# Kernel tuning notes

Hardware: AMD Instinct MI355X
Metric: run time of the kernel (lower is better)

## Reference

```python
import jax, jax.numpy as jnp
import numpy as np

B, S, D = 2, 4096, 768
H = 12
HD = D // H  # 64
INNER = 4 * D
EPS = 1e-5


def setup_inputs() -> dict:
    key = jax.random.key(0)
    ks = jax.random.split(key, 12)
    sd = 0.02
    # causal additive mask (GPT-2 style): 0 where allowed, -1e9 where masked
    causal = jnp.tril(jnp.ones((S, S), dtype=bool))
    attention_mask = jnp.where(causal, 0.0, -1e9).astype(jnp.float32)[None, None]
    return {
        "hidden_states": jax.random.normal(ks[0], (B, S, D), dtype=jnp.float32),
        "attention_mask": attention_mask,
        "ln1_g": jnp.ones((D,), jnp.float32),
        "ln1_b": jnp.zeros((D,), jnp.float32),
        "w_attn": jax.random.normal(ks[1], (D, 3 * D), jnp.float32) * sd,
        "b_attn": jnp.zeros((3 * D,), jnp.float32),
        "w_cproj": jax.random.normal(ks[2], (D, D), jnp.float32) * sd,
        "b_cproj": jnp.zeros((D,), jnp.float32),
        "ln2_g": jnp.ones((D,), jnp.float32),
        "ln2_b": jnp.zeros((D,), jnp.float32),
        "w_fc": jax.random.normal(ks[3], (D, INNER), jnp.float32) * sd,
        "b_fc": jnp.zeros((INNER,), jnp.float32),
        "w_fc_proj": jax.random.normal(ks[4], (INNER, D), jnp.float32) * sd,
        "b_fc_proj": jnp.zeros((D,), jnp.float32),
    }


def _layernorm(x, g, b):
    mu = jnp.mean(x, axis=-1, keepdims=True)
    var = jnp.mean(jnp.square(x - mu), axis=-1, keepdims=True)
    return (x - mu) * jax.lax.rsqrt(var + EPS) * g + b


def reference(hidden_states, attention_mask, ln1_g, ln1_b, w_attn, b_attn,
              w_cproj, b_cproj, ln2_g, ln2_b, w_fc, b_fc, w_fc_proj, b_fc_proj):
    residual = hidden_states
    x = _layernorm(hidden_states, ln1_g, ln1_b)
    # qkv projection
    qkv = x @ w_attn + b_attn                       # [B,S,3D]
    q, k, v = jnp.split(qkv, 3, axis=-1)
    q = q.reshape(B, S, H, HD).transpose(0, 2, 1, 3)  # [B,H,S,HD]
    k = k.reshape(B, S, H, HD).transpose(0, 2, 1, 3)
    v = v.reshape(B, S, H, HD).transpose(0, 2, 1, 3)
    scale = HD ** -0.5
    scores = jnp.einsum('bhqd,bhkd->bhqk', q, k) * scale + attention_mask
    attn = jax.nn.softmax(scores, axis=-1)
    ctx = jnp.einsum('bhqk,bhkd->bhqd', attn, v)    # [B,H,S,HD]
    ctx = ctx.transpose(0, 2, 1, 3).reshape(B, S, D)
    attn_out = ctx @ w_cproj + b_cproj
    h = attn_out + residual
    residual = h
    y = _layernorm(h, ln2_g, ln2_b)
    y = jax.nn.gelu(y @ w_fc + b_fc, approximate=False)  # nn.GELU default = exact
    y = y @ w_fc_proj + b_fc_proj
    return y + residual
```

## Files before the change

kernel.cpp:

```cpp
#include <hip/hip_runtime.h>
#include <hip/hip_bf16.h>


#define S_     4096
#define D_     768
#define H_     12
#define HD_    64
#define NB_    2
#define M_     (NB_*S_)
#define QKV_   (3*D_)
#define INNER_ 3072

typedef unsigned short u16;
typedef __attribute__((ext_vector_type(4))) float f32x4;
typedef __attribute__((ext_vector_type(8))) short s16x8;

__device__ __forceinline__ float bf2f(u16 h) {
    union { unsigned int u; float f; } c; c.u = ((unsigned int)h) << 16; return c.f;
}
__device__ __forceinline__ u16 f2bf(float f) {
    union { float f; unsigned int u; } c; c.f = f;
    return (u16)((c.u + 0x7fffu + ((c.u >> 16) & 1u)) >> 16);
}
__device__ __forceinline__ void storev(u16* p, float v) { *p = f2bf(v); }
__device__ __forceinline__ void storev(float* p, float v) { *p = v; }

__device__ __forceinline__ float fexp2(float x) {
#if __has_builtin(__builtin_amdgcn_exp2f)
    return __builtin_amdgcn_exp2f(x);
#else
    return __expf(x * 0.69314718056f);
#endif
}
__device__ __forceinline__ unsigned int packbf(float a, float b) {
    union { __hip_bfloat162 h; unsigned int u; } c;
    c.h = __float22bfloat162_rn(float2{a, b});
    return c.u;
}

__device__ __forceinline__ void gload_lds16(const u16* g, u16* l) {
    __builtin_amdgcn_global_load_lds((const __attribute__((address_space(1))) void*)g,
                                     (__attribute__((address_space(3))) void*)l, 16, 0, 0);
}

#define WAITVM(N) asm volatile("s_waitcnt vmcnt(" #N ")" ::: "memory")

template <typename IT, bool PERM>
__global__ __launch_bounds__(256) void transpose_kernel(const IT* __restrict__ in,
                                                        u16* __restrict__ out,
                                                        int ld_in, int ld_out) {
    __shared__ u16 tile[32][33];
    const int c0 = blockIdx.x * 32, r0 = blockIdx.y * 32;
    const int tx = threadIdx.x & 31, ty = threadIdx.x >> 5;
#pragma unroll
    for (int i = 0; i < 32; i += 8) {
        IT v = in[(size_t)(r0 + ty + i) * ld_in + c0 + tx];
        u16 bv;
        if constexpr (sizeof(IT) == 4) bv = f2bf((float)v); else bv = (u16)v;
        tile[ty + i][tx] = bv;
    }
    __syncthreads();
    int oc = r0 + tx;
    if constexpr (PERM) oc = (oc & ~63) | (((oc & 15) << 2) | ((oc >> 4) & 3));
#pragma unroll
    for (int i = 0; i < 32; i += 8)
        out[(size_t)(c0 + ty + i) * ld_out + oc] = tile[tx][ty + i];
}

__global__ __launch_bounds__(256) void ln_row(const float* __restrict__ x, const float* __restrict__ g,
                                              const float* __restrict__ bb, u16* __restrict__ y,
                                              unsigned int* ctr) {
    const int row = blockIdx.x;
    const int tid = threadIdx.x;
    if (ctr && row == 0 && tid == 0) *ctr = 0u;
    const float* xr = x + (size_t)row * D_;
    float v0 = xr[tid], v1 = xr[tid + 256], v2 = xr[tid + 512];
    float s = v0 + v1 + v2, s2 = v0 * v0 + v1 * v1 + v2 * v2;
#pragma unroll
    for (int d = 32; d >= 1; d >>= 1) { s += __shfl_xor(s, d, 64); s2 += __shfl_xor(s2, d, 64); }
    __shared__ float red[8];
    const int wave = tid >> 6, lane = tid & 63;
    if (lane == 0) { red[wave] = s; red[4 + wave] = s2; }
    __syncthreads();
    s = red[0] + red[1] + red[2] + red[3];
    s2 = red[4] + red[5] + red[6] + red[7];
    const float mu = s * (1.0f / D_);
    const float var = s2 * (1.0f / D_) - mu * mu;
    const float rstd = rsqrtf(var + 1e-5f);
    u16* yr = y + (size_t)row * D_;
    yr[tid]       = f2bf((v0 - mu) * rstd * g[tid]       + bb[tid]);
    yr[tid + 256] = f2bf((v1 - mu) * rstd * g[tid + 256] + bb[tid + 256]);
    yr[tid + 512] = f2bf((v2 - mu) * rstd * g[tid + 512] + bb[tid + 512]);
}

template <int EPI, typename OT>
__global__ __launch_bounds__(256) void gemm_bt(const u16* __restrict__ A, const u16* __restrict__ Bt,
                                               const float* __restrict__ bias, const float* res,
                                               OT* C, int M, int N, int K) {
    __shared__ u16 As[3][128 * 32];
    __shared__ u16 Bs[3][128 * 32];
    const int tid = threadIdx.x;
    const int wave = tid >> 6, lane = tid & 63;
    const int m0 = blockIdx.y << 7, n0 = blockIdx.x << 7;
    const int fr = lane & 15, quad = lane >> 4;

    const int srow = wave * 16 + (lane >> 2);
    const int scol = (lane & 3) * 8;
    const u16* ag0 = A + (size_t)(m0 + srow) * K + scol;
    const u16* ag1 = ag0 + (size_t)64 * K;
    const u16* bg0 = Bt + (size_t)(n0 + srow) * K + scol;
    const u16* bg1 = bg0 + (size_t)64 * K;

    auto STAGE = [&](int k0, int b) {
        gload_lds16(ag0 + k0, &As[b][wave * 512]);
        gload_lds16(ag1 + k0, &As[b][2048 + wave * 512]);
        gload_lds16(bg0 + k0, &Bs[b][wave * 512]);
        gload_lds16(bg1 + k0, &Bs[b][2048 + wave * 512]);
    };

    const f32x4 fz = {0.f, 0.f, 0.f, 0.f};
    f32x4 acc[4][4];
#pragma unroll
    for (int i = 0; i < 4; i++)
#pragma unroll
        for (int j = 0; j < 4; j++) acc[i][j] = fz;

    const int wm = wave & 1, wn = wave >> 1;
    const int a_off = (wm * 64 + fr) * 32 + quad * 8;
    const int b_off = (wn * 64 + fr) * 32 + quad * 8;

    const int nsteps = K >> 5;
    STAGE(0, 0);
    if (nsteps > 1) { STAGE(32, 1); WAITVM(4); } else { WAITVM(0); }
    __syncthreads();

    for (int t = 0; t < nsteps; t++) {
        if (t + 2 < nsteps) STAGE((t + 2) << 5, (t + 2) % 3);
        const u16* a_rd = &As[t % 3][a_off];
        const u16* b_rd = &Bs[t % 3][b_off];
        s16x8 af[4], bfr[4];
#pragma unroll
        for (int u = 0; u < 4; u++) {
            af[u]  = *(const s16x8*)(a_rd + u * 16 * 32);
            bfr[u] = *(const s16x8*)(b_rd + u * 16 * 32);
        }
#pragma unroll
        for (int mt = 0; mt < 4; mt++)
#pragma unroll
            for (int nt = 0; nt < 4; nt++)
                acc[mt][nt] = __builtin_amdgcn_mfma_f32_16x16x32_bf16(af[mt], bfr[nt], acc[mt][nt], 0, 0, 0);
        if (t + 2 < nsteps) { WAITVM(4); } else { WAITVM(0); }
        __syncthreads();
    }

    const int crow0 = m0 + wm * 64 + quad * 4;
    const int ccol0 = n0 + wn * 64 + fr;
#pragma unroll
    for (int nt = 0; nt < 4; nt++) {
        const int col = ccol0 + nt * 16;
        const float bv = bias[col];
#pragma unroll
        for (int mt = 0; mt < 4; mt++) {
#pragma unroll
            for (int r = 0; r < 4; r++) {
                const int row = crow0 + mt * 16 + r;
                float v = acc[mt][nt][r] + bv;
                if constexpr (EPI == 1) v = 0.5f * v * (1.0f + erff(v * 0.70710678118654752f));
                if constexpr (EPI == 2) v += res[(size_t)row * N + col];
                storev(&C[(size_t)row * N + col], v);
            }
        }
    }
}

template <int EPI, typename OT>
__global__ __launch_bounds__(256) void gemm_bt64(const u16* __restrict__ A, const u16* __restrict__ Bt,
                                                 const float* __restrict__ bias, const float* res,
                                                 OT* C, int M, int N, int K) {
    __shared__ u16 As[3][128 * 32];
    __shared__ u16 Bs[3][64 * 32];
    const int tid = threadIdx.x;
    const int wave = tid >> 6, lane = tid & 63;
    const int m0 = blockIdx.y << 7, n0 = blockIdx.x << 6;
    const int fr = lane & 15, quad = lane >> 4;

    const int srow = wave * 16 + (lane >> 2);
    const int scol = (lane & 3) * 8;
    const u16* ag0 = A + (size_t)(m0 + srow) * K + scol;
    const u16* ag1 = ag0 + (size_t)64 * K;
    const u16* bg0 = Bt + (size_t)(n0 + srow) * K + scol;

    auto STAGE = [&](int k0, int b) {
        gload_lds16(ag0 + k0, &As[b][wave * 512]);
        gload_lds16(ag1 + k0, &As[b][2048 + wave * 512]);
        gload_lds16(bg0 + k0, &Bs[b][wave * 512]);
    };

    const f32x4 fz = {0.f, 0.f, 0.f, 0.f};
    f32x4 acc[2][4];
#pragma unroll
    for (int i = 0; i < 2; i++)
#pragma unroll
        for (int j = 0; j < 4; j++) acc[i][j] = fz;

    const int a_off = (wave * 32 + fr) * 32 + quad * 8;
    const int b_off = fr * 32 + quad * 8;

    const int nsteps = K >> 5;
    STAGE(0, 0);
    if (nsteps > 1) { STAGE(32, 1); WAITVM(3); } else { WAITVM(0); }
    __syncthreads();

    for (int t = 0; t < nsteps; t++) {
        if (t + 2 < nsteps) STAGE((t + 2) << 5, (t + 2) % 3);
        const u16* a_rd = &As[t % 3][a_off];
        const u16* b_rd = &Bs[t % 3][b_off];
        s16x8 af[2], bfr[4];
#pragma unroll
        for (int u = 0; u < 2; u++) af[u] = *(const s16x8*)(a_rd + u * 16 * 32);
#pragma unroll
        for (int u = 0; u < 4; u++) bfr[u] = *(const s16x8*)(b_rd + u * 16 * 32);
#pragma unroll
        for (int mt = 0; mt < 2; mt++)
#pragma unroll
            for (int nt = 0; nt < 4; nt++)
                acc[mt][nt] = __builtin_amdgcn_mfma_f32_16x16x32_bf16(af[mt], bfr[nt], acc[mt][nt], 0, 0, 0);
        if (t + 2 < nsteps) { WAITVM(3); } else { WAITVM(0); }
        __syncthreads();
    }

    const int crow0 = m0 + wave * 32 + quad * 4;
    const int ccol0 = n0 + fr;
#pragma unroll
    for (int nt = 0; nt < 4; nt++) {
        const int col = ccol0 + nt * 16;
        const float bv = bias[col];
#pragma unroll
        for (int mt = 0; mt < 2; mt++) {
#pragma unroll
            for (int r = 0; r < 4; r++) {
                const int row = crow0 + mt * 16 + r;
                float v = acc[mt][nt][r] + bv;
                if constexpr (EPI == 1) v = 0.5f * v * (1.0f + erff(v * 0.70710678118654752f));
                if constexpr (EPI == 2) v += res[(size_t)row * N + col];
                storev(&C[(size_t)row * N + col], v);
            }
        }
    }
}

#define SCALE_  0.1803368801111f
#define PST_    72
#define NITEMS_ (32 * H_ * NB_)
#define NWORK_  512
__global__ __launch_bounds__(256, 2) void flash_attn(const u16* __restrict__ qkv, const u16* __restrict__ vt,
                                                     u16* __restrict__ ctx, unsigned int* __restrict__ ctr) {
    const int tid = threadIdx.x;
    const int wave = tid >> 6, lane = tid & 63;
    const int fr = lane & 15, quad = lane >> 4;

    __shared__ u16 Ks[3][64 * 64];
    __shared__ u16 Vs[3][64 * 64];
    __shared__ u16 Ps4[4][32 * PST_];
    __shared__ int item_sh;
    u16* Ps = Ps4[wave];

    const int rsub = lane >> 3;
    const int schunk = ((lane & 7) ^ rsub) << 3;
    const int lds_woff = (wave << 4) * 64;

    const f32x4 fz = {0.f, 0.f, 0.f, 0.f};
    s16x8 ones;
#pragma unroll
    for (int j = 0; j < 8; j++) ones[j] = (short)0x3F80;

    for (;;) {
        if (tid == 0) item_sh = (int)atomicAdd(ctr, 1u);
        __syncthreads();
        const int item = item_sh;
        if (item >= NITEMS_) return;

        const int strip = 31 - item / (H_ * NB_);
        const int hb = item % (H_ * NB_);
        const int h = hb % H_, b = hb / H_;
        const int q0 = strip << 7;
        const int qwv = q0 + (wave << 5);

        const u16* Qg  = qkv + ((size_t)b * S_ + qwv) * QKV_ + h * HD_;
        const u16* Kg  = qkv + (size_t)b * S_ * QKV_ + D_ + h * HD_;
        const u16* Vtg = vt + ((size_t)b * D_ + h * HD_) * S_;
        const u16* KgS = Kg + (size_t)((wave << 4) + rsub) * QKV_ + schunk;
        const u16* VgS = Vtg + (size_t)((wave << 4) + rsub) * S_ + schunk;

        auto STAGEF = [&](int t, int bf) {
            const u16* kg = KgS + (size_t)(t << 6) * QKV_;
            const u16* vg = VgS + (t << 6);
            gload_lds16(kg, &Ks[bf][lds_woff]);
            gload_lds16(kg + (size_t)8 * QKV_, &Ks[bf][lds_woff + 512]);
            gload_lds16(vg, &Vs[bf][lds_woff]);
            gload_lds16(vg + (size_t)8 * S_, &Vs[bf][lds_woff + 512]);
        };

        s16x8 qf[2][2];
#pragma unroll
        for (int mt = 0; mt < 2; mt++)
#pragma unroll
            for (int kk = 0; kk < 2; kk++)
                qf[mt][kk] = *(const s16x8*)(Qg + (size_t)(mt * 16 + fr) * QKV_ + kk * 32 + quad * 8);

        f32x4 o[2][4];
        f32x4 ls[2];
#pragma unroll
        for (int mt = 0; mt < 2; mt++) {
            ls[mt] = fz;
#pragma unroll
            for (int nt = 0; nt < 4; nt++) o[mt][nt] = fz;
        }

        const int ntw = (strip << 1) + 2;

        STAGEF(0, 0);
        STAGEF(1, 1);
        WAITVM(4);
        __syncthreads();

        for (int t = 0; t < ntw; t++) {
            const int k0 = t << 6;

            if (t + 2 < ntw) STAGEF(t + 2, (t + 2) % 3);

            if (k0 <= qwv + 31) {
                const u16* kb = Ks[t % 3];
                const u16* vb = Vs[t % 3];

                s16x8 kc[2][4];
#pragma unroll
                for (int kk = 0; kk < 2; kk++)
#pragma unroll
                    for (int nt = 0; nt < 4; nt++) {
                        const int row = nt * 16 + fr;
                        const int sl = ((kk * 4 + quad) ^ (fr & 7)) << 3;
                        kc[kk][nt] = *(const s16x8*)(kb + row * 64 + sl);
                    }

                f32x4 sc[2][4];
#pragma unroll
                for (int mt = 0; mt < 2; mt++)
#pragma unroll
                    for (int nt = 0; nt < 4; nt++) sc[mt][nt] = fz;
                __builtin_amdgcn_s_setprio(1);
#pragma unroll
                for (int kk = 0; kk < 2; kk++)
#pragma unroll
                    for (int mt = 0; mt < 2; mt++)
#pragma unroll
                        for (int nt = 0; nt < 4; nt++)
                            sc[mt][nt] = __builtin_amdgcn_mfma_f32_16x16x32_bf16(qf[mt][kk], kc[kk][nt], sc[mt][nt], 0, 0, 0);
                __builtin_amdgcn_s_setprio(0);

                const bool fast = (k0 + 63 <= qwv);
#pragma unroll
                for (int mt = 0; mt < 2; mt++) {
#pragma unroll
                    for (int r = 0; r < 4; r++) {
                        float s0 = sc[mt][0][r] * SCALE_;
                        float s1 = sc[mt][1][r] * SCALE_;
                        float s2 = sc[mt][2][r] * SCALE_;
                        float s3 = sc[mt][3][r] * SCALE_;
                        if (!fast) {
                            const int lim = (qwv + mt * 16 + quad * 4 + r) - k0;
                            if (fr      > lim) s0 = -1e30f;
                            if (fr + 16 > lim) s1 = -1e30f;
                            if (fr + 32 > lim) s2 = -1e30f;
                            if (fr + 48 > lim) s3 = -1e30f;
                        }
                        s0 = fexp2(s0); s1 = fexp2(s1); s2 = fexp2(s2); s3 = fexp2(s3);
                        const int prow = mt * 16 + quad * 4 + r;
                        *(uint2*)(Ps + prow * PST_ + fr * 4) = make_uint2(packbf(s0, s1), packbf(s2, s3));
                    }
                }

                s16x8 vf[2][4];
#pragma unroll
                for (int kk = 0; kk < 2; kk++)
#pragma unroll
                    for (int nt = 0; nt < 4; nt++) {
                        const int row = nt * 16 + fr;
                        const int sl = ((kk * 4 + quad) ^ (fr & 7)) << 3;
                        vf[kk][nt] = *(const s16x8*)(vb + row * 64 + sl);
                    }

                s16x8 pf[2][2];
#pragma unroll
                for (int mt = 0; mt < 2; mt++)
#pragma unroll
                    for (int kk = 0; kk < 2; kk++)
                        pf[mt][kk] = *(const s16x8*)(Ps + (mt * 16 + fr) * PST_ + kk * 32 + quad * 8);

                __builtin_amdgcn_s_setprio(1);
#pragma unroll
                for (int mt = 0; mt < 2; mt++) {
                    ls[mt] = __builtin_amdgcn_mfma_f32_16x16x32_bf16(pf[mt][0], ones, ls[mt], 0, 0, 0);
                    ls[mt] = __builtin_amdgcn_mfma_f32_16x16x32_bf16(pf[mt][1], ones, ls[mt], 0, 0, 0);
                }
#pragma unroll
                for (int kk = 0; kk < 2; kk++)
#pragma unroll
                    for (int mt = 0; mt < 2; mt++)
#pragma unroll
                        for (int nt = 0; nt < 4; nt++)
                            o[mt][nt] = __builtin_amdgcn_mfma_f32_16x16x32_bf16(pf[mt][kk], vf[kk][nt], o[mt][nt], 0, 0, 0);
                __builtin_amdgcn_s_setprio(0);
            }

            if (t + 2 < ntw) { WAITVM(4); } else { WAITVM(0); }
            __syncthreads();
        }

#pragma unroll
        for (int mt = 0; mt < 2; mt++) {
#pragma unroll
            for (int r = 0; r < 4; r++) {
                const int grow = qwv + mt * 16 + quad * 4 + r;
                const float inv = 1.0f / ls[mt][r];
                u16* crow = ctx + ((size_t)b * S_ + grow) * D_ + h * HD_ + fr;
#pragma unroll
                for (int nt = 0; nt < 4; nt++)
                    crow[nt * 16] = f2bf(o[mt][nt][r] * inv);
            }
        }
    }
}

extern "C" void kernel_launch(void* const* d_in, const int* in_sizes, int n_in,
                              void* d_out, int out_size, void* d_ws, size_t ws_size,
                              hipStream_t stream) {
    const float* hid    = (const float*)d_in[0];
    const float* ln1g   = (const float*)d_in[2];
    const float* ln1b   = (const float*)d_in[3];
    const float* w_attn = (const float*)d_in[4];
    const float* b_attn = (const float*)d_in[5];
    const float* w_cp   = (const float*)d_in[6];
    const float* b_cp   = (const float*)d_in[7];
    const float* ln2g   = (const float*)d_in[8];
    const float* ln2b   = (const float*)d_in[9];
    const float* w_fc   = (const float*)d_in[10];
    const float* b_fc   = (const float*)d_in[11];
    const float* w_fp   = (const float*)d_in[12];
    const float* b_fp   = (const float*)d_in[13];
    float* dout = (float*)d_out;

    unsigned int* ctr = (unsigned int*)d_out;

    u16* ws = (u16*)d_ws;
    u16* wTa  = ws; ws += (size_t)QKV_ * D_;
    u16* wTc  = ws; ws += (size_t)D_ * D_;
    u16* wTf  = ws; ws += (size_t)INNER_ * D_;
    u16* wTp  = ws; ws += (size_t)D_ * INNER_;
    u16* xln  = ws; ws += (size_t)M_ * D_;
    u16* qkvb = ws; ws += (size_t)M_ * QKV_;
    u16* vtb  = ws; ws += (size_t)NB_ * D_ * S_;
    u16* ctxb = xln;
    u16* yln  = xln;
    u16* act  = qkvb;

    dim3 blk(256);
    transpose_kernel<float, false><<<dim3(QKV_ / 32, D_ / 32), blk, 0, stream>>>(w_attn, wTa, QKV_, D_);
    transpose_kernel<float, false><<<dim3(D_ / 32, D_ / 32), blk, 0, stream>>>(w_cp, wTc, D_, D_);
    transpose_kernel<float, false><<<dim3(INNER_ / 32, D_ / 32), blk, 0, stream>>>(w_fc, wTf, INNER_, D_);
    transpose_kernel<float, false><<<dim3(D_ / 32, INNER_ / 32), blk, 0, stream>>>(w_fp, wTp, D_, INNER_);

    ln_row<<<M_, blk, 0, stream>>>(hid, ln1g, ln1b, xln, ctr);
    gemm_bt<0, u16><<<dim3(QKV_ / 128, M_ / 128), blk, 0, stream>>>(xln, wTa, b_attn, nullptr, qkvb, M_, QKV_, D_);

    transpose_kernel<u16, true><<<dim3(D_ / 32, S_ / 32), blk, 0, stream>>>(qkvb + 2 * D_, vtb, QKV_, S_);
    transpose_kernel<u16, true><<<dim3(D_ / 32, S_ / 32), blk, 0, stream>>>(qkvb + (size_t)S_ * QKV_ + 2 * D_,
                                                                            vtb + (size_t)D_ * S_, QKV_, S_);
    flash_attn<<<dim3(NWORK_), blk, 0, stream>>>(qkvb, vtb, ctxb, ctr);

    gemm_bt64<2, float><<<dim3(D_ / 64, M_ / 128), blk, 0, stream>>>(ctxb, wTc, b_cp, hid, dout, M_, D_, D_);
    ln_row<<<M_, blk, 0, stream>>>(dout, ln2g, ln2b, yln, nullptr);
    gemm_bt<1, u16><<<dim3(INNER_ / 128, M_ / 128), blk, 0, stream>>>(yln, wTf, b_fc, nullptr, act, M_, INNER_, D_);
    gemm_bt64<2, float><<<dim3(D_ / 64, M_ / 128), blk, 0, stream>>>(act, wTp, b_fp, dout, dout, M_, D_, INNER_);
}
```

Baseline: 527.8 us.

## Swizzle GEMM block order and switch flash attention to double buffering

The GEMM kernels remap the linear block id so that consecutive workgroups are spread in groups of eight across the tile grid, aiming for better L2 or XCD locality. Flash attention drops from a three-stage to a two-stage K/V LDS pipeline, which cuts shared memory use and could allow higher occupancy, but it now waits for all outstanding loads every iteration. The s_setprio hints around the MFMA blocks are also removed. Together these trade prefetch depth for lower LDS pressure and change the GEMM tile schedule.

```diff
diff --git a/kernel.cpp b/kernel.cpp
--- a/kernel.cpp
+++ b/kernel.cpp
@@ -101,8 +101,13 @@
     __shared__ u16 Bs[3][128 * 32];
     const int tid = threadIdx.x;
     const int wave = tid >> 6, lane = tid & 63;
-    const int m0 = blockIdx.y << 7, n0 = blockIdx.x << 7;
     const int fr = lane & 15, quad = lane >> 4;
+
+    const int nwg = (int)(gridDim.x * gridDim.y);
+    int id = (int)(blockIdx.y * gridDim.x + blockIdx.x);
+    id = (id & 7) * (nwg >> 3) + (id >> 3);
+    const int by = id / (int)gridDim.x, bx = id % (int)gridDim.x;
+    const int m0 = by << 7, n0 = bx << 7;
 
     const int srow = wave * 16 + (lane >> 2);
     const int scol = (lane & 3) * 8;
@@ -181,8 +186,13 @@
     __shared__ u16 Bs[3][64 * 32];
     const int tid = threadIdx.x;
     const int wave = tid >> 6, lane = tid & 63;
-    const int m0 = blockIdx.y << 7, n0 = blockIdx.x << 6;
     const int fr = lane & 15, quad = lane >> 4;
+
+    const int nwg = (int)(gridDim.x * gridDim.y);
+    int id = (int)(blockIdx.y * gridDim.x + blockIdx.x);
+    id = (id & 7) * (nwg >> 3) + (id >> 3);
+    const int by = id / (int)gridDim.x, bx = id % (int)gridDim.x;
+    const int m0 = by << 7, n0 = bx << 6;
 
     const int srow = wave * 16 + (lane >> 2);
     const int scol = (lane & 3) * 8;
@@ -259,15 +269,16 @@
     const int wave = tid >> 6, lane = tid & 63;
     const int fr = lane & 15, quad = lane >> 4;
 
-    __shared__ u16 Ks[3][64 * 64];
-    __shared__ u16 Vs[3][64 * 64];
+    __shared__ u16 Ks[2][64 * 64];
+    __shared__ u16 Vs[2][64 * 64];
     __shared__ u16 Ps4[4][32 * PST_];
     __shared__ int item_sh;
     u16* Ps = Ps4[wave];
 
     const int rsub = lane >> 3;
     const int schunk = ((lane & 7) ^ rsub) << 3;
-    const int lds_woff = (wave << 4) * 64;
+    u16* KlS0 = &Ks[0][(wave << 4) * 64];
+    u16* VlS0 = &Vs[0][(wave << 4) * 64];
 
     const f32x4 fz = {0.f, 0.f, 0.f, 0.f};
     s16x8 ones;
@@ -292,15 +303,6 @@
         const u16* KgS = Kg + (size_t)((wave << 4) + rsub) * QKV_ + schunk;
         const u16* VgS = Vtg + (size_t)((wave << 4) + rsub) * S_ + schunk;
 
-        auto STAGEF = [&](int t, int bf) {
-            const u16* kg = KgS + (size_t)(t << 6) * QKV_;
-            const u16* vg = VgS + (t << 6);
-            gload_lds16(kg, &Ks[bf][lds_woff]);
-            gload_lds16(kg + (size_t)8 * QKV_, &Ks[bf][lds_woff + 512]);
-            gload_lds16(vg, &Vs[bf][lds_woff]);
-            gload_lds16(vg + (size_t)8 * S_, &Vs[bf][lds_woff + 512]);
-        };
-
         s16x8 qf[2][2];
 #pragma unroll
         for (int mt = 0; mt < 2; mt++)
@@ -319,19 +321,32 @@
 
         const int ntw = (strip << 1) + 2;
 
-        STAGEF(0, 0);
-        STAGEF(1, 1);
-        WAITVM(4);
+        gload_lds16(KgS, KlS0);
+        gload_lds16(KgS + (size_t)8 * QKV_, KlS0 + 512);
+        gload_lds16(VgS, VlS0);
+        gload_lds16(VgS + (size_t)8 * S_, VlS0 + 512);
+        asm volatile("s_waitcnt vmcnt(0)" ::: "memory");
         __syncthreads();
 
+        int cur = 0;
         for (int t = 0; t < ntw; t++) {
             const int k0 = t << 6;
 
-            if (t + 2 < ntw) STAGEF(t + 2, (t + 2) % 3);
+            if (t + 1 < ntw) {
+                const int nb = cur ^ 1;
+                const u16* kg = KgS + (size_t)((t + 1) << 6) * QKV_;
+                const u16* vg = VgS + ((t + 1) << 6);
+                u16* kl = KlS0 + nb * (64 * 64);
+                u16* vl = VlS0 + nb * (64 * 64);
+                gload_lds16(kg, kl);
+                gload_lds16(kg + (size_t)8 * QKV_, kl + 512);
+                gload_lds16(vg, vl);
+                gload_lds16(vg + (size_t)8 * S_, vl + 512);
+            }
 
             if (k0 <= qwv + 31) {
-                const u16* kb = Ks[t % 3];
-                const u16* vb = Vs[t % 3];
+                const u16* kb = Ks[cur];
+                const u16* vb = Vs[cur];
 
                 s16x8 kc[2][4];
 #pragma unroll
@@ -348,7 +363,6 @@
                 for (int mt = 0; mt < 2; mt++)
 #pragma unroll
                     for (int nt = 0; nt < 4; nt++) sc[mt][nt] = fz;
-                __builtin_amdgcn_s_setprio(1);
 #pragma unroll
                 for (int kk = 0; kk < 2; kk++)
 #pragma unroll
@@ -356,7 +370,6 @@
 #pragma unroll
                         for (int nt = 0; nt < 4; nt++)
                             sc[mt][nt] = __builtin_amdgcn_mfma_f32_16x16x32_bf16(qf[mt][kk], kc[kk][nt], sc[mt][nt], 0, 0, 0);
-                __builtin_amdgcn_s_setprio(0);
 
                 const bool fast = (k0 + 63 <= qwv);
 #pragma unroll
@@ -397,7 +410,6 @@
                     for (int kk = 0; kk < 2; kk++)
                         pf[mt][kk] = *(const s16x8*)(Ps + (mt * 16 + fr) * PST_ + kk * 32 + quad * 8);
 
-                __builtin_amdgcn_s_setprio(1);
 #pragma unroll
                 for (int mt = 0; mt < 2; mt++) {
                     ls[mt] = __builtin_amdgcn_mfma_f32_16x16x32_bf16(pf[mt][0], ones, ls[mt], 0, 0, 0);
@@ -410,11 +422,11 @@
 #pragma unroll
                         for (int nt = 0; nt < 4; nt++)
                             o[mt][nt] = __builtin_amdgcn_mfma_f32_16x16x32_bf16(pf[mt][kk], vf[kk][nt], o[mt][nt], 0, 0, 0);
-                __builtin_amdgcn_s_setprio(0);
             }
 
-            if (t + 2 < ntw) { WAITVM(4); } else { WAITVM(0); }
+            asm volatile("s_waitcnt vmcnt(0)" ::: "memory");
             __syncthreads();
+            cur ^= 1;
         }
 
 #pragma unroll
```

Result: faster. 508.6 us, median of 3 (-3.6%).
